# Performance work log

Measured on AMD Instinct MI355X. Metric: run time of the kernel, lower is better.

Reference implementation:

```python
import jax, jax.numpy as jnp
import numpy as np

B, L, A, D, H = 128, 48, 16, 256, 128
NEG = 1e10


def l2norm(v, eps=1e-8):
    return v / (jnp.sqrt(jnp.sum(v * v, axis=-1, keepdims=True)) + eps)


def setup_inputs():
    key = jax.random.key(0)
    ks = jax.random.split(key, 6)
    x = jax.random.normal(ks[0], (B, L, A, D), jnp.float32)
    lengths = jax.random.randint(ks[1], (B,), 8, L + 1)
    lengths = lengths.at[0].set(L)  # forward assumes lengths.max() == L
    audio_masks = (jax.random.uniform(ks[2], (B, L, A, 1)) < 0.7).astype(jnp.float32)
    audio_masks = audio_masks.at[..., 0, :].set(1.0)  # at least one valid frame per word
    w_sem = jax.random.normal(ks[3], (D, D), jnp.float32) * 0.05   # Linear(D,D,bias=False).weight
    w1 = jax.random.normal(ks[4], (H, 2 * D), jnp.float32) * 0.05  # Linear(2D,H).weight
    b1 = jnp.zeros((H,), jnp.float32)
    w2 = jax.random.normal(ks[5], (1, H), jnp.float32) * 0.05      # Linear(H,1,bias=False).weight
    return {"x": x, "lengths": lengths, "audio_masks": audio_masks,
            "w_sem": w_sem, "w1": w1, "b1": b1, "w2": w2}


def _merge(arr, cv, idx):
    """update_with_mask with fixed-length arrays: new[j]=arr[j] (j<idx), cv (j==idx), arr[j+1] (j>idx).
    Trailing garbage slot is masked downstream by length masks."""
    shift = jnp.concatenate([arr[:, 1:], arr[:, -1:]], axis=1)
    extra = (1,) * (arr.ndim - 2)
    j = jnp.arange(arr.shape[1]).reshape((1, -1) + extra)
    ib = idx.reshape((-1, 1) + extra)
    return jnp.where(j < ib, arr, jnp.where(j == ib, jnp.expand_dims(cv, 1), shift))


def _forward(x, lengths, audio_masks, w_sem, w1, b1, w2):
    Bq, Lq = x.shape[0], x.shape[1]
    S = Lq - 1  # max_select_cnt (lengths.max() == Lq)
    # masked max over audio frames: [B,L,D]
    sem0 = jnp.max(jnp.einsum('blad,ed->blae', x, w_sem) - NEG * (1.0 - audio_masks), axis=-2)
    word_mask = (jnp.arange(Lq)[None, :] < lengths[:, None]).astype(x.dtype)
    out_word = sem0 * word_mask[..., None]
    pos = jnp.arange(Lq, dtype=jnp.int32)
    bounds0 = jnp.broadcast_to(pos, (Bq, Lq))
    posm1 = jnp.arange(Lq - 1)

    def gat(a, k):  # gather along axis 1 at per-batch index
        return jnp.take_along_axis(a, k.reshape((-1, 1) + (1,) * (a.ndim - 2)), axis=1)[:, 0]

    def step(carry, i):
        syn, sem, lb, rb = carry
        valid = jnp.clip(lengths - 1 - i, 0)               # merges still allowed per sentence
        masked = (posm1[None, :] >= valid[:, None]).astype(x.dtype)
        undone = (valid > 0).astype(x.dtype)[:, None]
        feats = jnp.concatenate([l2norm(syn[:, 1:]), l2norm(syn[:, :-1])], axis=-1)  # [B,L-1,2D]
        h = jax.nn.relu(jnp.einsum('bld,hd->blh', feats, w1) + b1)
        logits = jnp.einsum('blh,oh->blo', h, w2)[..., 0] - NEG * masked
        probs = jax.nn.softmax(logits, axis=1)
        idx = jnp.argmax(probs, axis=1).astype(jnp.int32)  # volatile=True (greedy) path
        tp = jnp.take_along_axis(probs, idx[:, None], axis=1)[:, 0]
        s_l, s_r = gat(sem, idx), gat(sem, idx + 1)
        feat = l2norm(s_l + s_r)
        spans = jnp.stack([gat(lb, idx), gat(rb, idx + 1)], axis=1)  # [B,2]
        syn_c = l2norm(gat(syn, idx) + gat(syn, idx + 1))
        carry = (_merge(syn, syn_c, idx), _merge(sem, feat, idx),
                 _merge(lb, spans[:, 0], idx), _merge(rb, spans[:, 1], idx))
        outs = (feat * undone, l2norm(s_l) * undone, l2norm(s_r) * undone, idx, tp, spans)
        return carry, outs

    _, (features, lefts, rights, tree_idx, tree_probs, span_bounds) = jax.lax.scan(
        step, (sem0, sem0, bounds0, bounds0), jnp.arange(S))
    return features, lefts, rights, out_word, tree_idx, tree_probs, span_bounds


def reference(x, lengths, audio_masks, w_sem, w1, b1, w2):
    return _forward(x, lengths, audio_masks, w_sem, w1, b1, w2)
```

## Files before the change

### kernel.cpp

```cpp
#include <hip/hip_runtime.h>
#include <math.h>

#define NEGC 1e10f
#define EPSF 1e-8f

#define NB 128
#define NL 48
#define NA 16
#define ND 256
#define NH 128
#define NS 47
#define PB_STRIDE (NL*ND)

#define WS_WT   0
#define WS_INVN 65536
#define WS_LOG  (65536+6144)
#define WS_PHYS (65536+12288)

#define O_FEAT  0
#define O_LEFT  1540096
#define O_RIGHT 3080192
#define O_WORD  4620288
#define O_TIDX  6193152
#define O_TP    6199168
#define O_SPAN  6205184

__global__ __launch_bounds__(256) void k_transpose(const float* __restrict__ w_sem,
                                                   float* __restrict__ ws) {
  int blk = blockIdx.x, t = threadIdx.x;
  ws[WS_WT + blk*256 + t] = w_sem[t*256 + blk];
}

__global__ __launch_bounds__(128) void k_sem0(const float* __restrict__ x,
                                              const int* __restrict__ lengths,
                                              const float* __restrict__ amask,
                                              float* __restrict__ ws,
                                              float* __restrict__ out) {
  __shared__ float xs[2*NA*128];
  __shared__ float pen[2*NA];
  int bl0 = blockIdx.x * 2;
  int t = threadIdx.x;
  int wv = t >> 6;
  int c = t & 63;
  int bl = bl0 + wv;
  int b = bl / NL, l = bl - b*NL;
  if (t < 2*NA) pen[t] = -NEGC * (1.0f - amask[(size_t)(bl0 + (t >> 4))*NA + (t & 15)]);
  float4* xs4 = (float4*)xs;
  const float* wt = ws + WS_WT;
  int e0 = c*4;
  float acc[NA][4];
#pragma unroll
  for (int a = 0; a < NA; ++a) { acc[a][0]=0.f; acc[a][1]=0.f; acc[a][2]=0.f; acc[a][3]=0.f; }
  bool va[NA];

  for (int p = 0; p < 2; ++p) {
    if (p) __syncthreads();
#pragma unroll
    for (int r = 0; r < 8; ++r) {
      int f = t + 128*r;
      int tile = f >> 9, rem = f & 511;
      int a = rem >> 5, dq = rem & 31;
      const float4* xg4 = (const float4*)(x + (size_t)(bl0 + tile)*(NA*ND));
      xs4[f] = xg4[a*64 + p*32 + dq];
    }
    __syncthreads();
    if (p == 0) {
#pragma unroll
      for (int a = 0; a < NA; ++a) va[a] = (pen[wv*NA + a] == 0.0f);
    }
    for (int d0 = 0; d0 < 128; d0 += 4) {
      const float* wrow = wt + (size_t)(p*128 + d0)*ND + e0;
      float4 wr0 = *(const float4*)(wrow);
      float4 wr1 = *(const float4*)(wrow + ND);
      float4 wr2 = *(const float4*)(wrow + 2*ND);
      float4 wr3 = *(const float4*)(wrow + 3*ND);
#pragma unroll
      for (int a = 0; a < NA; ++a) {
        if (va[a]) {
          float4 xa = xs4[wv*512 + a*32 + (d0 >> 2)];
          acc[a][0] = fmaf(xa.x, wr0.x, acc[a][0]);
          acc[a][1] = fmaf(xa.x, wr0.y, acc[a][1]);
          acc[a][2] = fmaf(xa.x, wr0.z, acc[a][2]);
          acc[a][3] = fmaf(xa.x, wr0.w, acc[a][3]);
          acc[a][0] = fmaf(xa.y, wr1.x, acc[a][0]);
          acc[a][1] = fmaf(xa.y, wr1.y, acc[a][1]);
          acc[a][2] = fmaf(xa.y, wr1.z, acc[a][2]);
          acc[a][3] = fmaf(xa.y, wr1.w, acc[a][3]);
          acc[a][0] = fmaf(xa.z, wr2.x, acc[a][0]);
          acc[a][1] = fmaf(xa.z, wr2.y, acc[a][1]);
          acc[a][2] = fmaf(xa.z, wr2.z, acc[a][2]);
          acc[a][3] = fmaf(xa.z, wr2.w, acc[a][3]);
          acc[a][0] = fmaf(xa.w, wr3.x, acc[a][0]);
          acc[a][1] = fmaf(xa.w, wr3.y, acc[a][1]);
          acc[a][2] = fmaf(xa.w, wr3.z, acc[a][2]);
          acc[a][3] = fmaf(xa.w, wr3.w, acc[a][3]);
        }
      }
    }
  }
  float m0 = -INFINITY, m1 = -INFINITY, m2 = -INFINITY, m3 = -INFINITY;
#pragma unroll
  for (int a = 0; a < NA; ++a) {
    if (va[a]) {
      m0 = fmaxf(m0, acc[a][0]);
      m1 = fmaxf(m1, acc[a][1]);
      m2 = fmaxf(m2, acc[a][2]);
      m3 = fmaxf(m3, acc[a][3]);
    }
  }
  float* prow = ws + WS_PHYS + (size_t)b*PB_STRIDE + l*ND;
  *(float4*)(prow + e0) = make_float4(m0, m1, m2, m3);
  float wm = (l < lengths[b]) ? 1.0f : 0.0f;
  *(float4*)(out + O_WORD + (size_t)bl*ND + e0) = make_float4(m0*wm, m1*wm, m2*wm, m3*wm);
  float s2 = m0*m0 + m1*m1 + m2*m2 + m3*m3;
#pragma unroll
  for (int off = 32; off; off >>= 1) s2 += __shfl_down(s2, off);
  if (c == 0) ws[WS_INVN + bl] = 1.0f / (sqrtf(s2) + EPSF);
}

__global__ __launch_bounds__(512, 1) void k_prelogits(float* __restrict__ ws,
                                                      const float* __restrict__ w1g,
                                                      const float* __restrict__ b1g,
                                                      const float* __restrict__ w2g) {
  __shared__ float rows[25*ND];
  __shared__ float part[4*8*NH];
  __shared__ float invl[25];
  __shared__ float b1s[NH];
  __shared__ float w2s[NH];
  int bid = blockIdx.x;
  int b = bid >> 1, h = bid & 1;
  int p0 = h*24;
  int np = h ? 23 : 24;
  int nrows = h ? 24 : 25;
  int t = threadIdx.x;
  int lane = t & 63, wv = t >> 6;
  int j = t & 127, q = t >> 7;

  float w1f[128];
  {
    const float4* wsrc = (const float4*)(w1g + (size_t)j*512 + q*128);
#pragma unroll
    for (int kk = 0; kk < 32; ++kk) {
      float4 v = wsrc[kk];
      w1f[4*kk+0] = v.x; w1f[4*kk+1] = v.y; w1f[4*kk+2] = v.z; w1f[4*kk+3] = v.w;
    }
  }
#pragma unroll
  for (int kk = 0; kk < 32; ++kk)
    asm volatile("" : "+v"(w1f[4*kk+0]), "+v"(w1f[4*kk+1]), "+v"(w1f[4*kk+2]), "+v"(w1f[4*kk+3]));

  if (t < NH) { b1s[t] = b1g[t]; w2s[t] = w2g[t]; }
  if (t < nrows) invl[t] = ws[WS_INVN + b*48 + p0 + t];
  {
    const float4* pg4 = (const float4*)(ws + WS_PHYS + (size_t)b*PB_STRIDE);
    float4* rows4 = (float4*)rows;
    int n4 = nrows * 64;
    for (int u = t; u < n4; u += 512) rows4[u] = pg4[p0*64 + u];
  }
  __syncthreads();

  for (int ct = 0; ct < 3; ++ct) {
#pragma unroll
    for (int c = 0; c < 8; ++c) {
      int pp = ct*8 + c;
      if (pp < np) {
        int rloc = (q < 2) ? pp + 1 : pp;
        const float4* rp4 = (const float4*)(rows + rloc*ND + (q & 1)*128);
        float ax = 0.f, ay = 0.f, az = 0.f, aw = 0.f;
#pragma unroll
        for (int kk = 0; kk < 32; ++kk) {
          float4 rv = rp4[kk];
          ax = fmaf(w1f[4*kk+0], rv.x, ax);
          ay = fmaf(w1f[4*kk+1], rv.y, ay);
          az = fmaf(w1f[4*kk+2], rv.z, az);
          aw = fmaf(w1f[4*kk+3], rv.w, aw);
        }
        part[(q*8 + c)*NH + j] = (ax + ay) + (az + aw);
      }
    }
    __syncthreads();
    int pp = ct*8 + wv;
    if (pp < np) {
      float inR = invl[pp + 1], inL = invl[pp];
      float pr0 = part[(0*8+wv)*NH + lane]      + part[(1*8+wv)*NH + lane];
      float pl0 = part[(2*8+wv)*NH + lane]      + part[(3*8+wv)*NH + lane];
      float pr1 = part[(0*8+wv)*NH + lane + 64] + part[(1*8+wv)*NH + lane + 64];
      float pl1 = part[(2*8+wv)*NH + lane + 64] + part[(3*8+wv)*NH + lane + 64];
      float h0 = fmaf(inR, pr0, fmaf(inL, pl0, b1s[lane]));
      float h1 = fmaf(inR, pr1, fmaf(inL, pl1, b1s[lane + 64]));
      h0 = fmaxf(h0, 0.f); h1 = fmaxf(h1, 0.f);
      float v = w2s[lane]*h0 + w2s[lane + 64]*h1;
#pragma unroll
      for (int off = 32; off; off >>= 1) v += __shfl_down(v, off);
      if (lane == 0) ws[WS_LOG + b*48 + p0 + pp] = v;
    }
    __syncthreads();
  }
}

__global__ __launch_bounds__(512, 1) void k_tree(const int* __restrict__ lengths,
                                                 float* __restrict__ ws,
                                                 const float* __restrict__ w1g,
                                                 const float* __restrict__ b1g,
                                                 const float* __restrict__ w2g,
                                                 float* __restrict__ out) {
  __shared__ float rows[NL*ND];
  __shared__ float part[8*NH];
  __shared__ float logits[48];
  __shared__ int physIdx[48];
  __shared__ int lbA[48];
  __shared__ int rbA[48];
  __shared__ float invn[48];
  __shared__ float b1s[NH];
  __shared__ float w2s[NH];
  __shared__ float red[8];
  __shared__ int s_idx, s_rL;
  __shared__ float s_tp, s_max;

  int b = blockIdx.x;
  int t = threadIdx.x;
  int lane = t & 63, wv = t >> 6;
  int j = t & 127, q = t >> 7;
  int len = lengths[b];

  float w1f[128];
  {
    const float4* wsrc = (const float4*)(w1g + (size_t)j*512 + q*128);
#pragma unroll
    for (int kk = 0; kk < 32; ++kk) {
      float4 v = wsrc[kk];
      w1f[4*kk+0] = v.x; w1f[4*kk+1] = v.y; w1f[4*kk+2] = v.z; w1f[4*kk+3] = v.w;
    }
  }
#pragma unroll
  for (int kk = 0; kk < 32; ++kk)
    asm volatile("" : "+v"(w1f[4*kk+0]), "+v"(w1f[4*kk+1]), "+v"(w1f[4*kk+2]), "+v"(w1f[4*kk+3]));

  if (t < NH) { b1s[t] = b1g[t]; w2s[t] = w2g[t]; }
  if (t < 48) { physIdx[t] = t; lbA[t] = t; rbA[t] = t; invn[t] = ws[WS_INVN + b*48 + t]; }
  if (t < 47) logits[t] = ws[WS_LOG + b*48 + t];
  {
    const float4* pg4 = (const float4*)(ws + WS_PHYS + (size_t)b*PB_STRIDE);
    float4* rows4 = (float4*)rows;
    for (int u = t; u < NL*64; u += 512) rows4[u] = pg4[u];
  }
  __syncthreads();

  int pidx = -1;
  for (int i = 0; i < NS; ++i) {
    int valid = len - 1 - i; if (valid < 0) valid = 0;
    if (i > 0 && t == 0)
      invn[s_rL] = 1.0f / (sqrtf(red[4]+red[5]+red[6]+red[7]) + EPSF);
    if (valid >= 2) {
      if (i > 0) {
        int pos0 = -1, pos1 = -1, np = 0;
        if (pidx > 0) { pos0 = pidx - 1; np = 1; }
        if (pidx <= valid - 1) { if (np) pos1 = pidx; else pos0 = pidx; ++np; }
        {
          int r = (q < 2) ? physIdx[pos0 + 1] : physIdx[pos0];
          const float4* rp4 = (const float4*)(rows + r*ND + (q & 1)*128);
          float ax = 0.f, ay = 0.f, az = 0.f, aw = 0.f;
#pragma unroll
          for (int kk = 0; kk < 32; ++kk) {
            float4 rv = rp4[kk];
            ax = fmaf(w1f[4*kk+0], rv.x, ax);
            ay = fmaf(w1f[4*kk+1], rv.y, ay);
            az = fmaf(w1f[4*kk+2], rv.z, az);
            aw = fmaf(w1f[4*kk+3], rv.w, aw);
          }
          part[(q*2 + 0)*NH + j] = (ax + ay) + (az + aw);
        }
        if (np > 1) {
          int r = (q < 2) ? physIdx[pos1 + 1] : physIdx[pos1];
          const float4* rp4 = (const float4*)(rows + r*ND + (q & 1)*128);
          float ax = 0.f, ay = 0.f, az = 0.f, aw = 0.f;
#pragma unroll
          for (int kk = 0; kk < 32; ++kk) {
            float4 rv = rp4[kk];
            ax = fmaf(w1f[4*kk+0], rv.x, ax);
            ay = fmaf(w1f[4*kk+1], rv.y, ay);
            az = fmaf(w1f[4*kk+2], rv.z, az);
            aw = fmaf(w1f[4*kk+3], rv.w, aw);
          }
          part[(q*2 + 1)*NH + j] = (ax + ay) + (az + aw);
        }
        __syncthreads();
        if (wv < np) {
          int p = (wv == 0) ? pos0 : pos1;
          int rR = physIdx[p + 1], rLL = physIdx[p];
          float inR = invn[rR], inL = invn[rLL];
          float pr0 = part[(0*2+wv)*NH + lane]      + part[(1*2+wv)*NH + lane];
          float pl0 = part[(2*2+wv)*NH + lane]      + part[(3*2+wv)*NH + lane];
          float pr1 = part[(0*2+wv)*NH + lane + 64] + part[(1*2+wv)*NH + lane + 64];
          float pl1 = part[(2*2+wv)*NH + lane + 64] + part[(3*2+wv)*NH + lane + 64];
          float h0 = fmaf(inR, pr0, fmaf(inL, pl0, b1s[lane]));
          float h1 = fmaf(inR, pr1, fmaf(inL, pl1, b1s[lane + 64]));
          h0 = fmaxf(h0, 0.f); h1 = fmaxf(h1, 0.f);
          float v = w2s[lane]*h0 + w2s[lane + 64]*h1;
#pragma unroll
          for (int off = 32; off; off >>= 1) v += __shfl_down(v, off);
          if (lane == 0) logits[p] = v;
        }
        __syncthreads();
      }
      if (wv == 0) {
        float v = (lane < valid) ? logits[lane] : -INFINITY;
        int bi = lane;
#pragma unroll
        for (int off = 32; off; off >>= 1) {
          float ov = __shfl_down(v, off);
          int  oi = __shfl_down(bi, off);
          if (ov > v || (ov == v && oi < bi)) { v = ov; bi = oi; }
        }
        if (lane == 0) { s_idx = bi; s_max = v; }
      }
    } else {
      if (t == 0) { s_idx = 0; s_tp = (valid == 1) ? 1.0f : (1.0f/47.0f); }
    }
    __syncthreads();
    int idx = s_idx;
    int rL = 0, rR = 0; float slv = 0.f, srv = 0.f, inL = 0.f, inR = 0.f, sumv = 0.f;
    if (t < ND) {
      rL = physIdx[idx]; rR = physIdx[idx + 1];
      slv = rows[rL*ND + t]; srv = rows[rR*ND + t];
      inL = invn[rL]; inR = invn[rR];
      sumv = slv + srv;
      float q2 = sumv * sumv;
#pragma unroll
      for (int off = 32; off; off >>= 1) q2 += __shfl_down(q2, off);
      if (lane == 0) red[wv] = q2;
    }
    int sp0 = 0, sp1 = 0;
    if (t == 0) { s_rL = rL; sp0 = lbA[idx]; sp1 = rbA[idx + 1]; }
    if (wv == 4 && valid >= 2) {
      float ee = (lane < valid) ? expf(logits[lane] - s_max) : 0.f;
#pragma unroll
      for (int off = 32; off; off >>= 1) ee += __shfl_down(ee, off);
      if (lane == 0) s_tp = 1.0f / ee;
    }
    int tt = t - 320;
    int pv = 0, lv = 0, rv_ = 0; float gv = 0.f;
    if (wv == 5 && tt < 47) { pv = physIdx[tt+1]; lv = lbA[tt+1]; rv_ = rbA[tt+1]; gv = logits[tt+1]; }
    __syncthreads();
    float undone = valid > 0 ? 1.0f : 0.0f;
    if (t < ND) {
      float invns = 1.0f / (sqrtf(red[0]+red[1]+red[2]+red[3]) + EPSF);
      float featv = sumv * invns;
      int ob = (i*NB + b)*ND + t;
      out[O_FEAT  + ob] = featv * undone;
      out[O_LEFT  + ob] = slv * inL * undone;
      out[O_RIGHT + ob] = srv * inR * undone;
      rows[rL*ND + t] = featv;
      float q3 = featv * featv;
#pragma unroll
      for (int off = 32; off; off >>= 1) q3 += __shfl_down(q3, off);
      if (lane == 0) red[4 + wv] = q3;
    }
    if (t == 0) {
      out[O_TIDX + i*NB + b] = (float)idx;
      out[O_TP   + i*NB + b] = s_tp;
      out[O_SPAN + (i*NB + b)*2 + 0] = (float)sp0;
      out[O_SPAN + (i*NB + b)*2 + 1] = (float)sp1;
    }
    if (wv == 5 && tt < 47) {
      if (tt > idx) { physIdx[tt] = pv; lbA[tt] = lv; logits[tt] = gv; }
      if (tt >= idx) rbA[tt] = rv_;
    }
    __syncthreads();
    pidx = idx;
  }
}

extern "C" void kernel_launch(void* const* d_in, const int* in_sizes, int n_in,
                              void* d_out, int out_size, void* d_ws, size_t ws_size,
                              hipStream_t stream) {
  const float* x      = (const float*)d_in[0];
  const int*   lengths= (const int*)  d_in[1];
  const float* amask  = (const float*)d_in[2];
  const float* w_sem  = (const float*)d_in[3];
  const float* w1     = (const float*)d_in[4];
  const float* b1     = (const float*)d_in[5];
  const float* w2     = (const float*)d_in[6];
  float* out = (float*)d_out;
  float* ws  = (float*)d_ws;

  k_transpose<<<dim3(256), dim3(256), 0, stream>>>(w_sem, ws);
  k_sem0<<<dim3(NB*NL/2), dim3(128), 0, stream>>>(x, lengths, amask, ws, out);
  k_prelogits<<<dim3(256), dim3(512), 0, stream>>>(ws, w1, b1, w2);
  k_tree<<<dim3(NB), dim3(512), 0, stream>>>(lengths, ws, w1, b1, w2, out);
}
```

Baseline: 353.6 us.

## Make every wave compute logits and argmax redundantly to cut per-step barriers

Each wave now computes the fresh logits, argmax and softmax denominator itself with shuffles instead of going through shared-memory broadcasts of idx, tp and max. This removes two of the five barriers per scan step. The remaining barriers become a lighter custom LDS-wait plus s_barrier. The logits compaction is folded into the same update step, with the fresh values substituted in. The cost is redundant ALU work in all 8 waves, and it relies on hand-written barrier semantics being correct.

```diff
diff --git a/kernel.cpp b/kernel.cpp
--- a/kernel.cpp
+++ b/kernel.cpp
@@ -24,6 +24,12 @@
 #define O_TIDX  6193152
 #define O_TP    6199168
 #define O_SPAN  6205184
+
+__device__ __forceinline__ void ldsbar() {
+  asm volatile("s_waitcnt lgkmcnt(0)" ::: "memory");
+  __builtin_amdgcn_s_barrier();
+  __builtin_amdgcn_sched_barrier(0);
+}
 
 __global__ __launch_bounds__(256) void k_transpose(const float* __restrict__ w_sem,
                                                    float* __restrict__ ws) {
@@ -214,8 +220,6 @@
   __shared__ float b1s[NH];
   __shared__ float w2s[NH];
   __shared__ float red[8];
-  __shared__ int s_idx, s_rL;
-  __shared__ float s_tp, s_max;
 
   int b = blockIdx.x;
   int t = threadIdx.x;
@@ -246,82 +250,99 @@
   }
   __syncthreads();
 
-  int pidx = -1;
+  int pidx = -1, prev_rL = -1;
   for (int i = 0; i < NS; ++i) {
     int valid = len - 1 - i; if (valid < 0) valid = 0;
     if (i > 0 && t == 0)
-      invn[s_rL] = 1.0f / (sqrtf(red[4]+red[5]+red[6]+red[7]) + EPSF);
+      invn[prev_rL] = 1.0f / (sqrtf(red[4]+red[5]+red[6]+red[7]) + EPSF);
+    int pos0 = -1, pos1 = -1, np = 0;
+    if (valid >= 2 && i > 0) {
+      if (pidx > 0) { pos0 = pidx - 1; np = 1; }
+      if (pidx <= valid - 1) { if (np) pos1 = pidx; else pos0 = pidx; ++np; }
+      {
+        int r = (q < 2) ? physIdx[pos0 + 1] : physIdx[pos0];
+        const float4* rp4 = (const float4*)(rows + r*ND + (q & 1)*128);
+        float ax = 0.f, ay = 0.f, az = 0.f, aw = 0.f;
+#pragma unroll
+        for (int kk = 0; kk < 32; ++kk) {
+          float4 rv = rp4[kk];
+          ax = fmaf(w1f[4*kk+0], rv.x, ax);
+          ay = fmaf(w1f[4*kk+1], rv.y, ay);
+          az = fmaf(w1f[4*kk+2], rv.z, az);
+          aw = fmaf(w1f[4*kk+3], rv.w, aw);
+        }
+        part[(q*2 + 0)*NH + j] = (ax + ay) + (az + aw);
+      }
+      if (np > 1) {
+        int r = (q < 2) ? physIdx[pos1 + 1] : physIdx[pos1];
+        const float4* rp4 = (const float4*)(rows + r*ND + (q & 1)*128);
+        float ax = 0.f, ay = 0.f, az = 0.f, aw = 0.f;
+#pragma unroll
+        for (int kk = 0; kk < 32; ++kk) {
+          float4 rv = rp4[kk];
+          ax = fmaf(w1f[4*kk+0], rv.x, ax);
+          ay = fmaf(w1f[4*kk+1], rv.y, ay);
+          az = fmaf(w1f[4*kk+2], rv.z, az);
+          aw = fmaf(w1f[4*kk+3], rv.w, aw);
+        }
+        part[(q*2 + 1)*NH + j] = (ax + ay) + (az + aw);
+      }
+    }
+    ldsbar();
+    int idx = 0; float tp = 0.f;
+    float fresh0 = 0.f, fresh1 = 0.f;
     if (valid >= 2) {
       if (i > 0) {
-        int pos0 = -1, pos1 = -1, np = 0;
-        if (pidx > 0) { pos0 = pidx - 1; np = 1; }
-        if (pidx <= valid - 1) { if (np) pos1 = pidx; else pos0 = pidx; ++np; }
-        {
-          int r = (q < 2) ? physIdx[pos0 + 1] : physIdx[pos0];
-          const float4* rp4 = (const float4*)(rows + r*ND + (q & 1)*128);
-          float ax = 0.f, ay = 0.f, az = 0.f, aw = 0.f;
-#pragma unroll
-          for (int kk = 0; kk < 32; ++kk) {
-            float4 rv = rp4[kk];
-            ax = fmaf(w1f[4*kk+0], rv.x, ax);
-            ay = fmaf(w1f[4*kk+1], rv.y, ay);
-            az = fmaf(w1f[4*kk+2], rv.z, az);
-            aw = fmaf(w1f[4*kk+3], rv.w, aw);
-          }
-          part[(q*2 + 0)*NH + j] = (ax + ay) + (az + aw);
+        float inR0 = invn[physIdx[pos0 + 1]], inL0 = invn[physIdx[pos0]];
+        float prA = part[0*NH + lane]      + part[2*NH + lane];
+        float plA = part[4*NH + lane]      + part[6*NH + lane];
+        float prB = part[0*NH + lane + 64] + part[2*NH + lane + 64];
+        float plB = part[4*NH + lane + 64] + part[6*NH + lane + 64];
+        float h0 = fmaf(inR0, prA, fmaf(inL0, plA, b1s[lane]));
+        float h1 = fmaf(inR0, prB, fmaf(inL0, plB, b1s[lane + 64]));
+        h0 = fmaxf(h0, 0.f); h1 = fmaxf(h1, 0.f);
+        float v0 = w2s[lane]*h0 + w2s[lane + 64]*h1;
+        float v1 = 0.f;
+        if (np > 1) {
+          float inR1 = invn[physIdx[pos1 + 1]], inL1 = invn[physIdx[pos1]];
+          float prA1 = part[1*NH + lane]      + part[3*NH + lane];
+          float plA1 = part[5*NH + lane]      + part[7*NH + lane];
+          float prB1 = part[1*NH + lane + 64] + part[3*NH + lane + 64];
+          float plB1 = part[5*NH + lane + 64] + part[7*NH + lane + 64];
+          float g0 = fmaf(inR1, prA1, fmaf(inL1, plA1, b1s[lane]));
+          float g1 = fmaf(inR1, prB1, fmaf(inL1, plB1, b1s[lane + 64]));
+          g0 = fmaxf(g0, 0.f); g1 = fmaxf(g1, 0.f);
+          v1 = w2s[lane]*g0 + w2s[lane + 64]*g1;
         }
-        if (np > 1) {
-          int r = (q < 2) ? physIdx[pos1 + 1] : physIdx[pos1];
-          const float4* rp4 = (const float4*)(rows + r*ND + (q & 1)*128);
-          float ax = 0.f, ay = 0.f, az = 0.f, aw = 0.f;
-#pragma unroll
-          for (int kk = 0; kk < 32; ++kk) {
-            float4 rv = rp4[kk];
-            ax = fmaf(w1f[4*kk+0], rv.x, ax);
-            ay = fmaf(w1f[4*kk+1], rv.y, ay);
-            az = fmaf(w1f[4*kk+2], rv.z, az);
-            aw = fmaf(w1f[4*kk+3], rv.w, aw);
-          }
-          part[(q*2 + 1)*NH + j] = (ax + ay) + (az + aw);
-        }
-        __syncthreads();
-        if (wv < np) {
-          int p = (wv == 0) ? pos0 : pos1;
-          int rR = physIdx[p + 1], rLL = physIdx[p];
-          float inR = invn[rR], inL = invn[rLL];
-          float pr0 = part[(0*2+wv)*NH + lane]      + part[(1*2+wv)*NH + lane];
-          float pl0 = part[(2*2+wv)*NH + lane]      + part[(3*2+wv)*NH + lane];
-          float pr1 = part[(0*2+wv)*NH + lane + 64] + part[(1*2+wv)*NH + lane + 64];
-          float pl1 = part[(2*2+wv)*NH + lane + 64] + part[(3*2+wv)*NH + lane + 64];
-          float h0 = fmaf(inR, pr0, fmaf(inL, pl0, b1s[lane]));
-          float h1 = fmaf(inR, pr1, fmaf(inL, pl1, b1s[lane + 64]));
-          h0 = fmaxf(h0, 0.f); h1 = fmaxf(h1, 0.f);
-          float v = w2s[lane]*h0 + w2s[lane + 64]*h1;
-#pragma unroll
-          for (int off = 32; off; off >>= 1) v += __shfl_down(v, off);
-          if (lane == 0) logits[p] = v;
-        }
-        __syncthreads();
-      }
+#pragma unroll
+        for (int off = 32; off; off >>= 1) { v0 += __shfl_down(v0, off); v1 += __shfl_down(v1, off); }
+        fresh0 = __shfl(v0, 0);
+        fresh1 = __shfl(v1, 0);
+      }
+      float ev = (lane < valid) ? logits[lane] : -INFINITY;
+      if (lane == pos0) ev = fresh0;
+      if (lane == pos1) ev = fresh1;
+      float v = ev; int bi = lane;
+#pragma unroll
+      for (int off = 32; off; off >>= 1) {
+        float ov = __shfl_down(v, off);
+        int  oi = __shfl_down(bi, off);
+        if (ov > v || (ov == v && oi < bi)) { v = ov; bi = oi; }
+      }
+      idx = __shfl(bi, 0);
+      float maxv = __shfl(v, 0);
       if (wv == 0) {
-        float v = (lane < valid) ? logits[lane] : -INFINITY;
-        int bi = lane;
-#pragma unroll
-        for (int off = 32; off; off >>= 1) {
-          float ov = __shfl_down(v, off);
-          int  oi = __shfl_down(bi, off);
-          if (ov > v || (ov == v && oi < bi)) { v = ov; bi = oi; }
-        }
-        if (lane == 0) { s_idx = bi; s_max = v; }
+        float ee = (lane < valid) ? expf(ev - maxv) : 0.f;
+#pragma unroll
+        for (int off = 32; off; off >>= 1) ee += __shfl_down(ee, off);
+        tp = 1.0f / ee;
       }
     } else {
-      if (t == 0) { s_idx = 0; s_tp = (valid == 1) ? 1.0f : (1.0f/47.0f); }
-    }
-    __syncthreads();
-    int idx = s_idx;
-    int rL = 0, rR = 0; float slv = 0.f, srv = 0.f, inL = 0.f, inR = 0.f, sumv = 0.f;
+      idx = 0; tp = (valid == 1) ? 1.0f : (1.0f/47.0f);
+    }
+    int rL = physIdx[idx], rR = physIdx[idx + 1];
+    float slv = 0.f, srv = 0.f, inL = 0.f, inR = 0.f, sumv = 0.f;
     if (t < ND) {
-      rL = physIdx[idx]; rR = physIdx[idx + 1];
       slv = rows[rL*ND + t]; srv = rows[rR*ND + t];
       inL = invn[rL]; inR = invn[rR];
       sumv = slv + srv;
@@ -330,18 +351,16 @@
       for (int off = 32; off; off >>= 1) q2 += __shfl_down(q2, off);
       if (lane == 0) red[wv] = q2;
     }
+    int pv = 0, lv = 0, rv_ = 0; float nlg = 0.f;
+    if (t < 47) {
+      pv = physIdx[t+1]; lv = lbA[t+1]; rv_ = rbA[t+1];
+      int src = (t > idx) ? t + 1 : t;
+      float raw = logits[src];
+      nlg = (src == pos0) ? fresh0 : (src == pos1) ? fresh1 : raw;
+    }
     int sp0 = 0, sp1 = 0;
-    if (t == 0) { s_rL = rL; sp0 = lbA[idx]; sp1 = rbA[idx + 1]; }
-    if (wv == 4 && valid >= 2) {
-      float ee = (lane < valid) ? expf(logits[lane] - s_max) : 0.f;
-#pragma unroll
-      for (int off = 32; off; off >>= 1) ee += __shfl_down(ee, off);
-      if (lane == 0) s_tp = 1.0f / ee;
-    }
-    int tt = t - 320;
-    int pv = 0, lv = 0, rv_ = 0; float gv = 0.f;
-    if (wv == 5 && tt < 47) { pv = physIdx[tt+1]; lv = lbA[tt+1]; rv_ = rbA[tt+1]; gv = logits[tt+1]; }
-    __syncthreads();
+    if (t == 0) { sp0 = lbA[idx]; sp1 = rbA[idx + 1]; }
+    ldsbar();
     float undone = valid > 0 ? 1.0f : 0.0f;
     if (t < ND) {
       float invns = 1.0f / (sqrtf(red[0]+red[1]+red[2]+red[3]) + EPSF);
@@ -358,16 +377,17 @@
     }
     if (t == 0) {
       out[O_TIDX + i*NB + b] = (float)idx;
-      out[O_TP   + i*NB + b] = s_tp;
+      out[O_TP   + i*NB + b] = tp;
       out[O_SPAN + (i*NB + b)*2 + 0] = (float)sp0;
       out[O_SPAN + (i*NB + b)*2 + 1] = (float)sp1;
     }
-    if (wv == 5 && tt < 47) {
-      if (tt > idx) { physIdx[tt] = pv; lbA[tt] = lv; logits[tt] = gv; }
-      if (tt >= idx) rbA[tt] = rv_;
-    }
-    __syncthreads();
-    pidx = idx;
+    if (t < 47) {
+      logits[t] = nlg;
+      if (t > idx) { physIdx[t] = pv; lbA[t] = lv; }
+      if (t >= idx) rbA[t] = rv_;
+    }
+    ldsbar();
+    pidx = idx; prev_rL = rL;
   }
 }
 
```

New measurement: 372.3 us. 1.05x slower.
